# Kernel optimization log

Hardware: AMD Instinct MI355X
Metric: run time of the kernel (lower is better)

Reference implementation:

```python
import jax, jax.numpy as jnp
import numpy as np

N_NODES = 100000
N_EDGES = 1600000
VOCAB = 1000
EMB = 128
HID = 256
N_GRAPHS = 128
N_LABELS = 2


def setup_inputs() -> dict:
    key = jax.random.key(0)
    ks = jax.random.split(key, 16)
    s = 0.05
    inp = {
        "x_ids": jax.random.randint(ks[0], (N_NODES,), 0, VOCAB),
        "edge_index": jax.random.randint(ks[1], (2, N_EDGES), 0, N_NODES),
        "batch": jnp.sort(jax.random.randint(ks[2], (N_NODES,), 0, N_GRAPHS)),
        "emb": jax.random.normal(ks[3], (VOCAB, EMB)) * s,
        "W0": jax.random.normal(ks[4], (EMB, HID)) * s,
        "b0": jnp.zeros((HID,)),
        "W1": jax.random.normal(ks[5], (HID, HID)) * s,
        "b1": jnp.zeros((HID,)),
        "W2": jax.random.normal(ks[6], (HID, HID)) * s,
        "b2": jnp.zeros((HID,)),
        "W3": jax.random.normal(ks[7], (HID, HID)) * s,
        "b3": jnp.zeros((HID,)),
        "Wc1": jax.random.normal(ks[8], (2 * HID, HID)) * s,
        "bc1": jnp.zeros((HID,)),
        "Wc2": jax.random.normal(ks[9], (HID, N_LABELS)) * s,
        "bc2": jnp.zeros((N_LABELS,)),
    }
    return inp


def _gcn_conv(x, W, b, src, dst, dis):
    # GCNConv with self-loops: out = D^-1/2 (A+I) D^-1/2 (x W) + b
    xw = x @ W                                   # [N, H]
    norm = dis[src] * dis[dst]                   # [E]
    out = jnp.zeros_like(xw).at[dst].add(xw[src] * norm[:, None])
    out = out + xw * (dis * dis)[:, None]        # self-loop term
    return out + b


def reference(x_ids, edge_index, batch, emb, W0, b0, W1, b1, W2, b2, W3, b3,
              Wc1, bc1, Wc2, bc2):
    src, dst = edge_index[0], edge_index[1]
    # degree (incl. self loop) is the same every layer -> compute once
    deg = jnp.zeros((N_NODES,), jnp.float32).at[dst].add(1.0) + 1.0
    dis = jax.lax.rsqrt(deg)

    x = emb[x_ids]                               # [N, EMB]
    for W, b in ((W0, b0), (W1, b1), (W2, b2), (W3, b3)):
        x = jax.nn.relu(_gcn_conv(x, W, b, src, dst, dis))
        # dropout: identity in eval mode

    counts = jax.ops.segment_sum(jnp.ones((N_NODES,), x.dtype), batch,
                                 num_segments=N_GRAPHS)
    mean_pool = jax.ops.segment_sum(x, batch, num_segments=N_GRAPHS)
    mean_pool = mean_pool / jnp.maximum(counts, 1.0)[:, None]
    max_pool = jax.ops.segment_max(x, batch, num_segments=N_GRAPHS)
    max_pool = jnp.where(counts[:, None] > 0, max_pool, 0.0)

    g = jnp.concatenate([mean_pool, max_pool], axis=1)  # [G, 2H]
    h = jax.nn.relu(g @ Wc1 + bc1)
    logits = h @ Wc2 + bc2                               # [G, 2]
    return logits
```

## Files before the change

kernel.cpp:

```cpp
#include <hip/hip_runtime.h>
#include <hip/hip_bf16.h>
#include <cstdint>
#include <cstddef>

#define N_NODES 100000
#define N_EDGES 1600000
#define EMBD 128
#define HID 256
#define N_GRAPHS 128
#define VOCAB 1000
#define NB_SCAN 98

typedef short bf16x8 __attribute__((ext_vector_type(8)));
typedef float f32x4 __attribute__((ext_vector_type(4)));
typedef float f32x2 __attribute__((ext_vector_type(2)));

__device__ inline unsigned short rne_bf16(float f) {
  unsigned u = __float_as_uint(f);
  return (unsigned short)((u + 0x7FFFu + ((u >> 16) & 1u)) >> 16);
}
__device__ inline float bf16_to_f32(unsigned short h) {
  return __uint_as_float(((unsigned)h) << 16);
}
__device__ inline void split_hl(float v, unsigned short& h, unsigned short& l) {
  h = rne_bf16(v);
  float hf = __uint_as_float(((unsigned)h) << 16);
  l = rne_bf16(v - hf);
}
__device__ inline f32x4 cvt4(uint2 v) {
  f32x4 r;
  r[0] = __uint_as_float(v.x << 16);
  r[1] = __uint_as_float(v.x & 0xFFFF0000u);
  r[2] = __uint_as_float(v.y << 16);
  r[3] = __uint_as_float(v.y & 0xFFFF0000u);
  return r;
}
__device__ inline f32x2 cvt2(unsigned v) {
  f32x2 r;
  r[0] = __uint_as_float(v << 16);
  r[1] = __uint_as_float(v & 0xFFFF0000u);
  return r;
}

__global__ void k_indeg(const int* __restrict__ dst, int* __restrict__ indeg) {
  int e = blockIdx.x * 256 + threadIdx.x;
  if (e < N_EDGES) atomicAdd(&indeg[dst[e]], 1);
}

__global__ __launch_bounds__(1024)
void k_scan1(const int* __restrict__ indeg, int* __restrict__ off, int* __restrict__ bsum,
             float* __restrict__ dis) {
  __shared__ int s[1024];
  const int tid = threadIdx.x;
  int i = blockIdx.x * 1024 + tid;
  int v = (i < N_NODES) ? indeg[i] : 0;
  if (i < N_NODES) dis[i] = rsqrtf((float)(v + 1));
  s[tid] = v; __syncthreads();
  #pragma unroll
  for (int ofs = 1; ofs < 1024; ofs <<= 1) {
    int t2 = (tid >= ofs) ? s[tid - ofs] : 0;
    __syncthreads();
    s[tid] += t2;
    __syncthreads();
  }
  if (i < N_NODES) off[i] = s[tid] - v;
  if (tid == 1023) bsum[blockIdx.x] = s[1023];
}

__global__ void k_scan2(int* __restrict__ bsum) {
  if (threadIdx.x == 0) {
    int a = 0;
    for (int i = 0; i < NB_SCAN; ++i) { int t = bsum[i]; bsum[i] = a; a += t; }
    bsum[NB_SCAN] = a;
  }
}

__global__ __launch_bounds__(1024)
void k_scan3(int* __restrict__ off, int* __restrict__ cur, const int* __restrict__ bsum) {
  int i = blockIdx.x * 1024 + threadIdx.x;
  if (i < N_NODES) { int v = off[i] + bsum[blockIdx.x]; off[i] = v; cur[i] = v; }
  if (i == 0) off[N_NODES] = bsum[NB_SCAN];
}

__global__ void k_fill(const int* __restrict__ src, const int* __restrict__ dst,
                       const int* __restrict__ ids, const float* __restrict__ dis,
                       int* __restrict__ cursor, int2* __restrict__ csre,
                       int2* __restrict__ csre0) {
  int e = blockIdx.x * 256 + threadIdx.x;
  if (e < N_EDGES) {
    int s = src[e];
    float ds = dis[s];
    int p = atomicAdd(&cursor[dst[e]], 1);
    csre[p]  = make_int2(s, __float_as_int(ds));
    csre0[p] = make_int2(ids[s], __float_as_int(ds));
  }
}

__global__ void k_prep(const float* __restrict__ emb, unsigned short* __restrict__ emb16,
                       const float* __restrict__ W0, unsigned short* __restrict__ w0h,
                       unsigned short* __restrict__ w0l,
                       const float* __restrict__ W1, unsigned short* __restrict__ w1h,
                       unsigned short* __restrict__ w1l,
                       const float* __restrict__ W2, unsigned short* __restrict__ w2h,
                       unsigned short* __restrict__ w2l,
                       const float* __restrict__ W3, unsigned short* __restrict__ w3h,
                       unsigned short* __restrict__ w3l) {
  int i = blockIdx.x * 256 + threadIdx.x;
  if (i < VOCAB * EMBD) { emb16[i] = rne_bf16(emb[i]); return; }
  i -= VOCAB * EMBD;
  unsigned short h, l;
  if (i < EMBD * HID) {
    int k = i >> 8, n = i & 255;
    split_hl(W0[i], h, l);
    w0h[n * EMBD + k] = h; w0l[n * EMBD + k] = l;
    return;
  }
  i -= EMBD * HID;
  if (i >= 3 * HID * HID) return;
  int w = i >> 16, j = i & 65535;
  const float* Ws = (w == 0) ? W1 : (w == 1) ? W2 : W3;
  unsigned short* th = (w == 0) ? w1h : (w == 1) ? w2h : w3h;
  unsigned short* tl = (w == 0) ? w1l : (w == 1) ? w2l : w3l;
  int k = j >> 8, n = j & 255;
  split_hl(Ws[j], h, l);
  th[n * HID + k] = h; tl[n * HID + k] = l;
}

__global__ __launch_bounds__(256)
void k_agg0(const unsigned short* __restrict__ emb16, const int* __restrict__ ids,
            const float* __restrict__ dis, const int* __restrict__ off,
            const int2* __restrict__ csre0, unsigned short* __restrict__ aggA) {
  const int lane = threadIdx.x & 63;
  const int node = blockIdx.x * 4 + (threadIdx.x >> 6);
  const float di = dis[node];
  unsigned sv = *((const unsigned*)(emb16 + (size_t)ids[node] * EMBD) + lane);
  f32x2 a0 = di * cvt2(sv);
  f32x2 a1 = (f32x2)0.f, a2 = (f32x2)0.f, a3 = (f32x2)0.f;
  const int e0 = off[node], e1 = off[node + 1];
  int e = e0;
  for (; e + 4 <= e1; e += 4) {
    int2 c0 = csre0[e], c1 = csre0[e + 1], c2 = csre0[e + 2], c3 = csre0[e + 3];
    unsigned v0 = *((const unsigned*)(emb16 + (size_t)c0.x * EMBD) + lane);
    unsigned v1 = *((const unsigned*)(emb16 + (size_t)c1.x * EMBD) + lane);
    unsigned v2 = *((const unsigned*)(emb16 + (size_t)c2.x * EMBD) + lane);
    unsigned v3 = *((const unsigned*)(emb16 + (size_t)c3.x * EMBD) + lane);
    a0 += __int_as_float(c0.y) * cvt2(v0);
    a1 += __int_as_float(c1.y) * cvt2(v1);
    a2 += __int_as_float(c2.y) * cvt2(v2);
    a3 += __int_as_float(c3.y) * cvt2(v3);
  }
  for (; e < e1; ++e) {
    int2 c0 = csre0[e];
    unsigned v0 = *((const unsigned*)(emb16 + (size_t)c0.x * EMBD) + lane);
    a0 += __int_as_float(c0.y) * cvt2(v0);
  }
  f32x2 r = di * ((a0 + a1) + (a2 + a3));
  size_t base = (size_t)node * EMBD + lane * 2;
  *(ushort2*)&aggA[base] = make_ushort2(rne_bf16(r[0]), rne_bf16(r[1]));
}

__global__ __launch_bounds__(256)
void k_agg16(const unsigned short* __restrict__ y16, const float* __restrict__ dis,
             const int* __restrict__ off, const int2* __restrict__ csre,
             unsigned short* __restrict__ aggA) {
  const int lane = threadIdx.x & 63;
  const int node = blockIdx.x * 4 + (threadIdx.x >> 6);
  const float di = dis[node];
  uint2 sv = *((const uint2*)(y16 + (size_t)node * HID) + lane);
  f32x4 a0 = di * cvt4(sv);
  f32x4 a1 = (f32x4)0.f, a2 = (f32x4)0.f, a3 = (f32x4)0.f;
  const int e0 = off[node], e1 = off[node + 1];
  int e = e0;
  for (; e + 8 <= e1; e += 8) {
    int2 c0 = csre[e],     c1 = csre[e + 1], c2 = csre[e + 2], c3 = csre[e + 3];
    int2 c4 = csre[e + 4], c5 = csre[e + 5], c6 = csre[e + 6], c7 = csre[e + 7];
    uint2 v0 = *((const uint2*)(y16 + (size_t)c0.x * HID) + lane);
    uint2 v1 = *((const uint2*)(y16 + (size_t)c1.x * HID) + lane);
    uint2 v2 = *((const uint2*)(y16 + (size_t)c2.x * HID) + lane);
    uint2 v3 = *((const uint2*)(y16 + (size_t)c3.x * HID) + lane);
    uint2 v4 = *((const uint2*)(y16 + (size_t)c4.x * HID) + lane);
    uint2 v5 = *((const uint2*)(y16 + (size_t)c5.x * HID) + lane);
    uint2 v6 = *((const uint2*)(y16 + (size_t)c6.x * HID) + lane);
    uint2 v7 = *((const uint2*)(y16 + (size_t)c7.x * HID) + lane);
    a0 += __int_as_float(c0.y) * cvt4(v0);
    a1 += __int_as_float(c1.y) * cvt4(v1);
    a2 += __int_as_float(c2.y) * cvt4(v2);
    a3 += __int_as_float(c3.y) * cvt4(v3);
    a0 += __int_as_float(c4.y) * cvt4(v4);
    a1 += __int_as_float(c5.y) * cvt4(v5);
    a2 += __int_as_float(c6.y) * cvt4(v6);
    a3 += __int_as_float(c7.y) * cvt4(v7);
  }
  for (; e + 4 <= e1; e += 4) {
    int2 c0 = csre[e], c1 = csre[e + 1], c2 = csre[e + 2], c3 = csre[e + 3];
    uint2 v0 = *((const uint2*)(y16 + (size_t)c0.x * HID) + lane);
    uint2 v1 = *((const uint2*)(y16 + (size_t)c1.x * HID) + lane);
    uint2 v2 = *((const uint2*)(y16 + (size_t)c2.x * HID) + lane);
    uint2 v3 = *((const uint2*)(y16 + (size_t)c3.x * HID) + lane);
    a0 += __int_as_float(c0.y) * cvt4(v0);
    a1 += __int_as_float(c1.y) * cvt4(v1);
    a2 += __int_as_float(c2.y) * cvt4(v2);
    a3 += __int_as_float(c3.y) * cvt4(v3);
  }
  for (; e < e1; ++e) {
    int2 c0 = csre[e];
    uint2 v0 = *((const uint2*)(y16 + (size_t)c0.x * HID) + lane);
    a0 += __int_as_float(c0.y) * cvt4(v0);
  }
  f32x4 r = di * ((a0 + a1) + (a2 + a3));
  size_t base = (size_t)node * HID + lane * 4;
  *(ushort4*)&aggA[base] = make_ushort4(rne_bf16(r[0]), rne_bf16(r[1]),
                                        rne_bf16(r[2]), rne_bf16(r[3]));
}

__device__ inline void gl_lds16(const void* g, void* l) {
  __builtin_amdgcn_global_load_lds((const __attribute__((address_space(1))) unsigned int*)g,
                                   (__attribute__((address_space(3))) unsigned int*)l,
                                   16, 0, 0);
}

template<int K>
__global__ __launch_bounds__(256)
void k_gemm_mfma(const unsigned short* __restrict__ Ah,
                 const unsigned short* __restrict__ Wh, const unsigned short* __restrict__ Wl,
                 const float* __restrict__ bias, unsigned short* __restrict__ C16) {
  __shared__ unsigned short sA[2][128 * 32];
  __shared__ unsigned short sBh[2][128 * 32];
  __shared__ unsigned short sBl[2][128 * 32];
  const int tid = threadIdx.x;
  const int lane = tid & 63;
  const int wid = tid >> 6;
  const int wr = wid >> 1, wc = wid & 1;
  const int row0 = blockIdx.x * 128;
  const int col0 = blockIdx.y * 128;
  const int cl = lane & 15;
  const int sl = lane >> 4;
  const int nt = K / 32;

  f32x4 acc[4][4];
  #pragma unroll
  for (int i = 0; i < 4; ++i)
    #pragma unroll
    for (int j = 0; j < 4; ++j) acc[i][j] = (f32x4)0.f;

  auto stage = [&](int b, int kt) {
    #pragma unroll
    for (int q = 0; q < 2; ++q) {
      int c = (wid * 2 + q) * 64 + lane;
      int row = c >> 2, slot = c & 3;
      int ss = slot ^ (row & 3);
      int ga = row0 + row; if (ga > N_NODES - 1) ga = N_NODES - 1;
      size_t aoff = (size_t)ga * K + kt + ss * 8;
      gl_lds16(Ah + aoff, &sA[b][(wid * 2 + q) * 512]);
      size_t boff = (size_t)(col0 + row) * K + kt + ss * 8;
      gl_lds16(Wh + boff, &sBh[b][(wid * 2 + q) * 512]);
      gl_lds16(Wl + boff, &sBl[b][(wid * 2 + q) * 512]);
    }
  };

  stage(0, 0);
  __syncthreads();

  for (int t = 0; t < nt; ++t) {
    const int cur = t & 1;
    if (t + 1 < nt) stage(cur ^ 1, (t + 1) * 32);

    bf16x8 fa[4], fbh[4], fbl[4];
    #pragma unroll
    for (int f = 0; f < 4; ++f) {
      int ra = wr * 64 + f * 16 + cl;
      int oa = ra * 32 + ((sl ^ (ra & 3)) << 3);
      fa[f] = *(const bf16x8*)&sA[cur][oa];
      int rb = wc * 64 + f * 16 + cl;
      int ob = rb * 32 + ((sl ^ (rb & 3)) << 3);
      fbh[f] = *(const bf16x8*)&sBh[cur][ob];
      fbl[f] = *(const bf16x8*)&sBl[cur][ob];
    }
    #pragma unroll
    for (int i = 0; i < 4; ++i)
      #pragma unroll
      for (int j = 0; j < 4; ++j) {
        acc[i][j] = __builtin_amdgcn_mfma_f32_16x16x32_bf16(fa[i], fbh[j], acc[i][j], 0, 0, 0);
        acc[i][j] = __builtin_amdgcn_mfma_f32_16x16x32_bf16(fa[i], fbl[j], acc[i][j], 0, 0, 0);
      }
    __syncthreads();
  }

  #pragma unroll
  for (int j = 0; j < 4; ++j) {
    int gn = col0 + wc * 64 + j * 16 + cl;
    float bn = bias[gn];
    #pragma unroll
    for (int i = 0; i < 4; ++i) {
      f32x4 v = acc[i][j];
      #pragma unroll
      for (int r = 0; r < 4; ++r) {
        int gm = row0 + wr * 64 + i * 16 + sl * 4 + r;
        if (gm < N_NODES) C16[(size_t)gm * HID + gn] = rne_bf16(fmaxf(v[r] + bn, 0.f));
      }
    }
  }
}

__device__ inline int lower_bound_i(const int* a, int n, int v) {
  int lo = 0, hi = n;
  while (lo < hi) { int m = (lo + hi) >> 1; if (a[m] < v) lo = m + 1; else hi = m; }
  return lo;
}

__global__ __launch_bounds__(256)
void k_pool(const unsigned short* __restrict__ y16, const int* __restrict__ batch,
            float* __restrict__ gsum, float* __restrict__ gmax) {
  const int gi = blockIdx.x, ck = blockIdx.y, t = threadIdx.x;
  const int start = lower_bound_i(batch, N_NODES, gi);
  const int end   = lower_bound_i(batch, N_NODES, gi + 1);
  const int len = end - start;
  const int c0 = start + (len * ck) / 4;
  const int c1 = start + (len * (ck + 1)) / 4;
  float sum = 0.f, mx = 0.f;
  #pragma unroll 4
  for (int n = c0; n < c1; ++n) {
    float v = bf16_to_f32(y16[(size_t)n * HID + t]);
    sum += v; mx = fmaxf(mx, v);
  }
  if (c0 < c1) {
    atomicAdd(&gsum[gi * HID + t], sum);
    atomicMax((int*)&gmax[gi * HID + t], __float_as_int(mx));
  }
}

__global__ __launch_bounds__(256)
void k_cls(const float* __restrict__ gsum, const float* __restrict__ gmax,
           const int* __restrict__ batch,
           const float* __restrict__ Wc1, const float* __restrict__ bc1,
           const float* __restrict__ Wc2, const float* __restrict__ bc2,
           float* __restrict__ out) {
  const int gi = blockIdx.x, t = threadIdx.x;
  __shared__ float sg[512];
  __shared__ float sh[256];
  const int start = lower_bound_i(batch, N_NODES, gi);
  const int end   = lower_bound_i(batch, N_NODES, gi + 1);
  const float rcnt = 1.f / (float)((end - start) > 0 ? (end - start) : 1);
  sg[t] = gsum[gi * HID + t] * rcnt;
  sg[256 + t] = gmax[gi * HID + t];
  __syncthreads();
  float a = bc1[t];
  #pragma unroll 8
  for (int k = 0; k < 512; ++k) a = fmaf(sg[k], Wc1[k * HID + t], a);
  sh[t] = fmaxf(a, 0.f);
  __syncthreads();
  if (t < 2) {
    float o = bc2[t];
    for (int k = 0; k < 256; ++k) o = fmaf(sh[k], Wc2[k * 2 + t], o);
    out[gi * 2 + t] = o;
  }
}

extern "C" void kernel_launch(void* const* d_in, const int* in_sizes, int n_in,
                              void* d_out, int out_size, void* d_ws, size_t ws_size,
                              hipStream_t stream) {
  const int*   x_ids = (const int*)d_in[0];
  const int*   ei    = (const int*)d_in[1];
  const int*   batch = (const int*)d_in[2];
  const float* emb   = (const float*)d_in[3];
  const float* W0 = (const float*)d_in[4];  const float* b0 = (const float*)d_in[5];
  const float* W1 = (const float*)d_in[6];  const float* b1 = (const float*)d_in[7];
  const float* W2 = (const float*)d_in[8];  const float* b2 = (const float*)d_in[9];
  const float* W3 = (const float*)d_in[10]; const float* b3 = (const float*)d_in[11];
  const float* Wc1 = (const float*)d_in[12]; const float* bc1 = (const float*)d_in[13];
  const float* Wc2 = (const float*)d_in[14]; const float* bc2 = (const float*)d_in[15];
  float* out = (float*)d_out;
  const int* src = ei;
  const int* dst = ei + N_EDGES;

  char* ws = (char*)d_ws;
  size_t o = 0;
  auto alloc = [&](size_t bytes) -> char* {
    char* p = ws + o; o += (bytes + 255) & ~(size_t)255; return p;
  };
  unsigned short* y16  = (unsigned short*)alloc((size_t)N_NODES * HID * 2);
  unsigned short* aggA = (unsigned short*)alloc((size_t)N_NODES * HID * 2);
  float* dis   = (float*)alloc((size_t)N_NODES * 4);
  int*   indeg = (int*)  alloc((size_t)N_NODES * 4);
  int*   off   = (int*)  alloc((size_t)(N_NODES + 1) * 4);
  int*   cur   = (int*)  alloc((size_t)(N_NODES + 1) * 4);
  int*   bsum  = (int*)  alloc((size_t)(NB_SCAN + 1) * 4);
  int2*  csre  = (int2*) alloc((size_t)N_EDGES * 8);
  int2*  csre0 = (int2*) alloc((size_t)N_EDGES * 8);
  unsigned short* emb16 = (unsigned short*)alloc((size_t)VOCAB * EMBD * 2);
  unsigned short* wbuf  = (unsigned short*)alloc((size_t)458752 * 2);
  float* gsum  = (float*)alloc((size_t)N_GRAPHS * HID * 4);
  float* gmax  = (float*)alloc((size_t)N_GRAPHS * HID * 4);
  (void)ws_size; (void)in_sizes; (void)n_in; (void)out_size;

  unsigned short* wt0h = wbuf;            unsigned short* wt0l = wbuf + 32768;
  unsigned short* wt1h = wbuf + 65536;    unsigned short* wt1l = wbuf + 131072;
  unsigned short* wt2h = wbuf + 196608;   unsigned short* wt2l = wbuf + 262144;
  unsigned short* wt3h = wbuf + 327680;   unsigned short* wt3l = wbuf + 393216;

  hipMemsetAsync(indeg, 0, (size_t)N_NODES * 4, stream);
  hipMemsetAsync(gsum, 0, (size_t)N_GRAPHS * HID * 4 * 2 + 256, stream);
  k_indeg<<<N_EDGES / 256, 256, 0, stream>>>(dst, indeg);
  k_scan1<<<NB_SCAN, 1024, 0, stream>>>(indeg, off, bsum, dis);
  k_scan2<<<1, 64, 0, stream>>>(bsum);
  k_scan3<<<NB_SCAN, 1024, 0, stream>>>(off, cur, bsum);
  k_fill<<<N_EDGES / 256, 256, 0, stream>>>(src, dst, x_ids, dis, cur, csre, csre0);
  k_prep<<<(VOCAB * EMBD + EMBD * HID + 3 * HID * HID + 255) / 256, 256, 0, stream>>>(
      emb, emb16, W0, wt0h, wt0l, W1, wt1h, wt1l, W2, wt2h, wt2l, W3, wt3h, wt3l);

  dim3 ggrid((N_NODES + 127) / 128, 2);
  k_agg0<<<N_NODES / 4, 256, 0, stream>>>(emb16, x_ids, dis, off, csre0, aggA);
  k_gemm_mfma<128><<<ggrid, 256, 0, stream>>>(aggA, wt0h, wt0l, b0, y16);
  k_agg16<<<N_NODES / 4, 256, 0, stream>>>(y16, dis, off, csre, aggA);
  k_gemm_mfma<256><<<ggrid, 256, 0, stream>>>(aggA, wt1h, wt1l, b1, y16);
  k_agg16<<<N_NODES / 4, 256, 0, stream>>>(y16, dis, off, csre, aggA);
  k_gemm_mfma<256><<<ggrid, 256, 0, stream>>>(aggA, wt2h, wt2l, b2, y16);
  k_agg16<<<N_NODES / 4, 256, 0, stream>>>(y16, dis, off, csre, aggA);
  k_gemm_mfma<256><<<ggrid, 256, 0, stream>>>(aggA, wt3h, wt3l, b3, y16);

  dim3 pgrid(N_GRAPHS, 4);
  k_pool<<<pgrid, 256, 0, stream>>>(y16, batch, gsum, gmax);
  k_cls<<<N_GRAPHS, 256, 0, stream>>>(gsum, gmax, batch, Wc1, bc1, Wc2, bc2, out);
}
```

Baseline: 950.6 us.

## Drop duplicate csre0 edge list, parallelize block-sum scan, trim agg16 unroll

The fill kernel no longer writes a second edge array of token ids. The first-layer aggregation instead looks up ids[src] indirectly, which removes 12.8MB of scattered writes and a 12.8MB read but adds a dependent gather per edge. The single-threaded block-sum scan becomes a 128-thread shared-memory scan. The 8-wide unrolled loop in agg16 is removed, so fewer gathers are in flight per wave.

```diff
diff --git a/kernel.cpp b/kernel.cpp
--- a/kernel.cpp
+++ b/kernel.cpp
@@ -68,11 +68,19 @@
 }
 
 __global__ void k_scan2(int* __restrict__ bsum) {
-  if (threadIdx.x == 0) {
-    int a = 0;
-    for (int i = 0; i < NB_SCAN; ++i) { int t = bsum[i]; bsum[i] = a; a += t; }
-    bsum[NB_SCAN] = a;
-  }
+  __shared__ int s[128];
+  const int t = threadIdx.x;
+  int v = (t < NB_SCAN) ? bsum[t] : 0;
+  s[t] = v; __syncthreads();
+  #pragma unroll
+  for (int ofs = 1; ofs < 128; ofs <<= 1) {
+    int x = (t >= ofs) ? s[t - ofs] : 0;
+    __syncthreads();
+    s[t] += x;
+    __syncthreads();
+  }
+  if (t < NB_SCAN) bsum[t] = s[t] - v;
+  if (t == 127) bsum[NB_SCAN] = s[127];
 }
 
 __global__ __launch_bounds__(1024)
@@ -83,16 +91,14 @@
 }
 
 __global__ void k_fill(const int* __restrict__ src, const int* __restrict__ dst,
-                       const int* __restrict__ ids, const float* __restrict__ dis,
-                       int* __restrict__ cursor, int2* __restrict__ csre,
-                       int2* __restrict__ csre0) {
+                       const float* __restrict__ dis,
+                       int* __restrict__ cursor, int2* __restrict__ csre) {
   int e = blockIdx.x * 256 + threadIdx.x;
   if (e < N_EDGES) {
     int s = src[e];
     float ds = dis[s];
     int p = atomicAdd(&cursor[dst[e]], 1);
-    csre[p]  = make_int2(s, __float_as_int(ds));
-    csre0[p] = make_int2(ids[s], __float_as_int(ds));
+    csre[p] = make_int2(s, __float_as_int(ds));
   }
 }
 
@@ -129,7 +135,7 @@
 __global__ __launch_bounds__(256)
 void k_agg0(const unsigned short* __restrict__ emb16, const int* __restrict__ ids,
             const float* __restrict__ dis, const int* __restrict__ off,
-            const int2* __restrict__ csre0, unsigned short* __restrict__ aggA) {
+            const int2* __restrict__ csre, unsigned short* __restrict__ aggA) {
   const int lane = threadIdx.x & 63;
   const int node = blockIdx.x * 4 + (threadIdx.x >> 6);
   const float di = dis[node];
@@ -139,19 +145,20 @@
   const int e0 = off[node], e1 = off[node + 1];
   int e = e0;
   for (; e + 4 <= e1; e += 4) {
-    int2 c0 = csre0[e], c1 = csre0[e + 1], c2 = csre0[e + 2], c3 = csre0[e + 3];
-    unsigned v0 = *((const unsigned*)(emb16 + (size_t)c0.x * EMBD) + lane);
-    unsigned v1 = *((const unsigned*)(emb16 + (size_t)c1.x * EMBD) + lane);
-    unsigned v2 = *((const unsigned*)(emb16 + (size_t)c2.x * EMBD) + lane);
-    unsigned v3 = *((const unsigned*)(emb16 + (size_t)c3.x * EMBD) + lane);
+    int2 c0 = csre[e], c1 = csre[e + 1], c2 = csre[e + 2], c3 = csre[e + 3];
+    int i0 = ids[c0.x], i1 = ids[c1.x], i2 = ids[c2.x], i3 = ids[c3.x];
+    unsigned v0 = *((const unsigned*)(emb16 + (size_t)i0 * EMBD) + lane);
+    unsigned v1 = *((const unsigned*)(emb16 + (size_t)i1 * EMBD) + lane);
+    unsigned v2 = *((const unsigned*)(emb16 + (size_t)i2 * EMBD) + lane);
+    unsigned v3 = *((const unsigned*)(emb16 + (size_t)i3 * EMBD) + lane);
     a0 += __int_as_float(c0.y) * cvt2(v0);
     a1 += __int_as_float(c1.y) * cvt2(v1);
     a2 += __int_as_float(c2.y) * cvt2(v2);
     a3 += __int_as_float(c3.y) * cvt2(v3);
   }
   for (; e < e1; ++e) {
-    int2 c0 = csre0[e];
-    unsigned v0 = *((const unsigned*)(emb16 + (size_t)c0.x * EMBD) + lane);
+    int2 c0 = csre[e];
+    unsigned v0 = *((const unsigned*)(emb16 + (size_t)ids[c0.x] * EMBD) + lane);
     a0 += __int_as_float(c0.y) * cvt2(v0);
   }
   f32x2 r = di * ((a0 + a1) + (a2 + a3));
@@ -171,26 +178,6 @@
   f32x4 a1 = (f32x4)0.f, a2 = (f32x4)0.f, a3 = (f32x4)0.f;
   const int e0 = off[node], e1 = off[node + 1];
   int e = e0;
-  for (; e + 8 <= e1; e += 8) {
-    int2 c0 = csre[e],     c1 = csre[e + 1], c2 = csre[e + 2], c3 = csre[e + 3];
-    int2 c4 = csre[e + 4], c5 = csre[e + 5], c6 = csre[e + 6], c7 = csre[e + 7];
-    uint2 v0 = *((const uint2*)(y16 + (size_t)c0.x * HID) + lane);
-    uint2 v1 = *((const uint2*)(y16 + (size_t)c1.x * HID) + lane);
-    uint2 v2 = *((const uint2*)(y16 + (size_t)c2.x * HID) + lane);
-    uint2 v3 = *((const uint2*)(y16 + (size_t)c3.x * HID) + lane);
-    uint2 v4 = *((const uint2*)(y16 + (size_t)c4.x * HID) + lane);
-    uint2 v5 = *((const uint2*)(y16 + (size_t)c5.x * HID) + lane);
-    uint2 v6 = *((const uint2*)(y16 + (size_t)c6.x * HID) + lane);
-    uint2 v7 = *((const uint2*)(y16 + (size_t)c7.x * HID) + lane);
-    a0 += __int_as_float(c0.y) * cvt4(v0);
-    a1 += __int_as_float(c1.y) * cvt4(v1);
-    a2 += __int_as_float(c2.y) * cvt4(v2);
-    a3 += __int_as_float(c3.y) * cvt4(v3);
-    a0 += __int_as_float(c4.y) * cvt4(v4);
-    a1 += __int_as_float(c5.y) * cvt4(v5);
-    a2 += __int_as_float(c6.y) * cvt4(v6);
-    a3 += __int_as_float(c7.y) * cvt4(v7);
-  }
   for (; e + 4 <= e1; e += 4) {
     int2 c0 = csre[e], c1 = csre[e + 1], c2 = csre[e + 2], c3 = csre[e + 3];
     uint2 v0 = *((const uint2*)(y16 + (size_t)c0.x * HID) + lane);
@@ -386,7 +373,6 @@
   int*   cur   = (int*)  alloc((size_t)(N_NODES + 1) * 4);
   int*   bsum  = (int*)  alloc((size_t)(NB_SCAN + 1) * 4);
   int2*  csre  = (int2*) alloc((size_t)N_EDGES * 8);
-  int2*  csre0 = (int2*) alloc((size_t)N_EDGES * 8);
   unsigned short* emb16 = (unsigned short*)alloc((size_t)VOCAB * EMBD * 2);
   unsigned short* wbuf  = (unsigned short*)alloc((size_t)458752 * 2);
   float* gsum  = (float*)alloc((size_t)N_GRAPHS * HID * 4);
@@ -399,17 +385,17 @@
   unsigned short* wt3h = wbuf + 327680;   unsigned short* wt3l = wbuf + 393216;
 
   hipMemsetAsync(indeg, 0, (size_t)N_NODES * 4, stream);
-  hipMemsetAsync(gsum, 0, (size_t)N_GRAPHS * HID * 4 * 2 + 256, stream);
+  hipMemsetAsync(gsum, 0, (size_t)N_GRAPHS * HID * 4 * 2, stream);
   k_indeg<<<N_EDGES / 256, 256, 0, stream>>>(dst, indeg);
   k_scan1<<<NB_SCAN, 1024, 0, stream>>>(indeg, off, bsum, dis);
-  k_scan2<<<1, 64, 0, stream>>>(bsum);
+  k_scan2<<<1, 128, 0, stream>>>(bsum);
   k_scan3<<<NB_SCAN, 1024, 0, stream>>>(off, cur, bsum);
-  k_fill<<<N_EDGES / 256, 256, 0, stream>>>(src, dst, x_ids, dis, cur, csre, csre0);
+  k_fill<<<N_EDGES / 256, 256, 0, stream>>>(src, dst, dis, cur, csre);
   k_prep<<<(VOCAB * EMBD + EMBD * HID + 3 * HID * HID + 255) / 256, 256, 0, stream>>>(
       emb, emb16, W0, wt0h, wt0l, W1, wt1h, wt1l, W2, wt2h, wt2l, W3, wt3h, wt3l);
 
   dim3 ggrid((N_NODES + 127) / 128, 2);
-  k_agg0<<<N_NODES / 4, 256, 0, stream>>>(emb16, x_ids, dis, off, csre0, aggA);
+  k_agg0<<<N_NODES / 4, 256, 0, stream>>>(emb16, x_ids, dis, off, csre, aggA);
   k_gemm_mfma<128><<<ggrid, 256, 0, stream>>>(aggA, wt0h, wt0l, b0, y16);
   k_agg16<<<N_NODES / 4, 256, 0, stream>>>(y16, dis, off, csre, aggA);
   k_gemm_mfma<256><<<ggrid, 256, 0, stream>>>(aggA, wt1h, wt1l, b1, y16);
```

Measured after the change: 976.9 us. 1.03x slower.
